# Kernel tuning notes

Measured on AMD Instinct MI355X. Metric: run time of the kernel, lower is better.

Reference implementation:

```python
import jax, jax.numpy as jnp
import numpy as np

N_NODES = 50000
N_EDGES = 800000
B, W, D, OUT = 2, 128, 64, 128


def setup_inputs() -> dict:
    key = jax.random.key(0)
    ks = jax.random.split(key, 8)
    s = lambda k, shape, fan: jax.random.normal(k, shape, dtype=jnp.float32) / np.sqrt(fan)
    return {
        "x": jax.random.normal(ks[0], (B, N_NODES, W), dtype=jnp.float32),
        "embeddings": jax.random.normal(ks[1], (N_NODES, D), dtype=jnp.float32),
        "edge_index": jax.random.randint(ks[2], (2, N_EDGES), 0, N_NODES, dtype=jnp.int64),
        "Wq": s(ks[3], (D, D), D),
        "Wk": s(ks[4], (D, D), D),
        "v": s(ks[5], (D,), D),
        "fcW": s(ks[6], (OUT, 2 * W), 2 * W),
        "fcb": jnp.zeros((OUT,), dtype=jnp.float32),
    }


def reference(x, embeddings, edge_index, Wq, Wk, v, fcW, fcb):
    B_, N, W_ = x.shape
    src, dst = edge_index[0], edge_index[1]

    # Project once on nodes, then gather per edge (same math as gather-then-linear).
    e_q = embeddings @ Wq.T        # [N, D]
    e_k = embeddings @ Wk.T        # [N, D]
    score = jnp.tanh(e_q[src] + e_k[dst]) @ v   # [E]

    # Scatter-softmax over destination nodes.
    max_vals = jax.ops.segment_max(score, dst, num_segments=N)   # [N], -inf for empty
    exp_src = jnp.exp(score - max_vals[dst])                     # [E]
    sum_exp = jax.ops.segment_sum(exp_src, dst, num_segments=N)  # [N]
    attn = exp_src / (sum_exp[dst] + 1e-8)                       # [E]

    # Weighted scatter-add aggregation of source features.
    weighted = x[:, src, :] * attn[None, :, None]                # [B, E, W]
    agg = jax.ops.segment_sum(jnp.swapaxes(weighted, 0, 1), dst, num_segments=N)  # [N, B, W]
    agg = jnp.swapaxes(agg, 0, 1)                                # [B, N, W]

    out = jnp.concatenate([x, agg], axis=-1) @ fcW.T + fcb       # [B, N, OUT]
    return jax.nn.relu(out)
```

## Files before the change

### kernel.cpp

```cpp
#include <hip/hip_runtime.h>
#include <hip/hip_bf16.h>
#include <math.h>

#define N_NODES 50000
#define N_EDGES 800000
#define BB 2
#define WFEAT 128
#define DD 64
#define OUTD 128
#define NROWS (BB * N_NODES)
#define SCAN_B 256
#define NBLK ((N_NODES + SCAN_B - 1) / SCAN_B)

#define CVTX_B 6250
#define CVTW_B 16
#define HIST_B 3125
#define PREP_B (CVTX_B + CVTW_B + HIST_B)
#define PROJ_TB ((N_NODES + 127) / 128)

typedef __attribute__((ext_vector_type(8))) short bf16x8;
typedef __attribute__((ext_vector_type(4))) float f32x4;
typedef __attribute__((ext_vector_type(2))) float f32x2;
typedef __attribute__((ext_vector_type(8))) unsigned short ushort8;

#define PRESCALE 2.8853900817779268f
#define L2E 1.4426950408889634f

static __device__ __forceinline__ unsigned short f2bf(float f) {
    __hip_bfloat16 h = __float2bfloat16(f);
    return *reinterpret_cast<unsigned short*>(&h);
}
static __device__ __forceinline__ float bf_lo(unsigned int w) {
    return __uint_as_float(w << 16);
}
static __device__ __forceinline__ float bf_hi(unsigned int w) {
    return __uint_as_float(w & 0xFFFF0000u);
}
static __device__ __forceinline__ f32x2 up2(unsigned int w) {
    f32x2 r;
    r.x = __uint_as_float(w << 16);
    r.y = __uint_as_float(w & 0xFFFF0000u);
    return r;
}
static __device__ __forceinline__ float exp2_hw(float x) {
    float r;
    asm("v_exp_f32 %0, %1" : "=v"(r) : "v"(x));
    return r;
}

__global__ __launch_bounds__(256) void prep_kernel(const float* __restrict__ x,
                                                   unsigned short* __restrict__ xb,
                                                   const float* __restrict__ fcW,
                                                   unsigned short* __restrict__ fcWb,
                                                   const int* __restrict__ dstp,
                                                   int* __restrict__ deg,
                                                   int* __restrict__ posin) {
    int bid = blockIdx.x;
    int tid = threadIdx.x;
    if (bid < CVTX_B) {
        int t = bid * 256 + tid;
        const float4* in4 = (const float4*)x;
        float4 a = in4[2 * t], b = in4[2 * t + 1];
        ushort8 o;
        o[0] = f2bf(a.x); o[1] = f2bf(a.y); o[2] = f2bf(a.z); o[3] = f2bf(a.w);
        o[4] = f2bf(b.x); o[5] = f2bf(b.y); o[6] = f2bf(b.z); o[7] = f2bf(b.w);
        *reinterpret_cast<ushort8*>(&xb[8 * t]) = o;
    } else if (bid < CVTX_B + CVTW_B) {
        int t = (bid - CVTX_B) * 256 + tid;
        const float4* in4 = (const float4*)fcW;
        float4 a = in4[2 * t], b = in4[2 * t + 1];
        ushort8 o;
        o[0] = f2bf(a.x); o[1] = f2bf(a.y); o[2] = f2bf(a.z); o[3] = f2bf(a.w);
        o[4] = f2bf(b.x); o[5] = f2bf(b.y); o[6] = f2bf(b.z); o[7] = f2bf(b.w);
        *reinterpret_cast<ushort8*>(&fcWb[8 * t]) = o;
    } else {
        int e = (bid - CVTX_B - CVTW_B) * 256 + tid;
        int d = dstp[e];
        posin[e] = atomicAdd(&deg[d], 1);
    }
}

__global__ __launch_bounds__(256) void proj_mfma(const float* __restrict__ emb,
                                                 const float* __restrict__ Wq,
                                                 const float* __restrict__ Wk,
                                                 unsigned short* __restrict__ eqb,
                                                 unsigned short* __restrict__ ekb) {
    __shared__ unsigned short As[128 * 64];
    __shared__ unsigned short Bs[128 * 64];
    int tid = threadIdx.x;
    int wave = tid >> 6, lane = tid & 63;
    int wm = wave >> 1, wn = wave & 1;
    int row0 = blockIdx.x * 128;

#pragma unroll
    for (int c = 0; c < 4; ++c) {
        int idx = (c * 256 + tid) * 8;
        int r = idx >> 6, k = idx & 63;
        int byte = (r * 128 + k * 2) ^ ((r & 7) << 4);

        int node = row0 + r;
        ushort8 o = {};
        if (node < N_NODES) {
            const float4* p = (const float4*)(emb + (size_t)node * DD + k);
            float4 a = p[0], b = p[1];
            o[0] = f2bf(a.x); o[1] = f2bf(a.y); o[2] = f2bf(a.z); o[3] = f2bf(a.w);
            o[4] = f2bf(b.x); o[5] = f2bf(b.y); o[6] = f2bf(b.z); o[7] = f2bf(b.w);
        }
        *reinterpret_cast<ushort8*>(reinterpret_cast<char*>(As) + byte) = o;

        const float* wsrc = (r < 64) ? (Wq + r * DD + k) : (Wk + (r - 64) * DD + k);
        float4 wa = *(const float4*)wsrc, wb = *((const float4*)wsrc + 1);
        ushort8 ow;
        ow[0] = f2bf(wa.x); ow[1] = f2bf(wa.y); ow[2] = f2bf(wa.z); ow[3] = f2bf(wa.w);
        ow[4] = f2bf(wb.x); ow[5] = f2bf(wb.y); ow[6] = f2bf(wb.z); ow[7] = f2bf(wb.w);
        *reinterpret_cast<ushort8*>(reinterpret_cast<char*>(Bs) + byte) = ow;
    }
    __syncthreads();

    f32x4 acc[4][4] = {};
#pragma unroll
    for (int kk = 0; kk < 2; ++kk) {
        bf16x8 a[4], b[4];
#pragma unroll
        for (int m = 0; m < 4; ++m) {
            int r = wm * 64 + m * 16 + (lane & 15);
            int k = kk * 32 + (lane >> 4) * 8;
            int byte = (r * 128 + k * 2) ^ ((r & 7) << 4);
            a[m] = *reinterpret_cast<bf16x8*>(reinterpret_cast<char*>(As) + byte);
        }
#pragma unroll
        for (int n = 0; n < 4; ++n) {
            int cn = wn * 64 + n * 16 + (lane & 15);
            int k = kk * 32 + (lane >> 4) * 8;
            int byte = (cn * 128 + k * 2) ^ ((cn & 7) << 4);
            b[n] = *reinterpret_cast<bf16x8*>(reinterpret_cast<char*>(Bs) + byte);
        }
#pragma unroll
        for (int m = 0; m < 4; ++m)
#pragma unroll
            for (int n = 0; n < 4; ++n)
                acc[m][n] = __builtin_amdgcn_mfma_f32_16x16x32_bf16(a[m], b[n], acc[m][n], 0, 0, 0);
    }

#pragma unroll
    for (int m = 0; m < 4; ++m) {
#pragma unroll
        for (int n = 0; n < 4; ++n) {
            int col = wn * 64 + n * 16 + (lane & 15);
#pragma unroll
            for (int j = 0; j < 4; ++j) {
                int row = row0 + wm * 64 + m * 16 + (lane >> 4) * 4 + j;
                if (row < N_NODES) {
                    unsigned short val = f2bf(PRESCALE * acc[m][n][j]);
                    if (col < 64) eqb[(size_t)row * DD + col] = val;
                    else          ekb[(size_t)row * DD + col - 64] = val;
                }
            }
        }
    }
}

__global__ void scan_reduce(const int* __restrict__ deg, int* __restrict__ bsum) {
    __shared__ int sh[SCAN_B];
    int i = blockIdx.x * SCAN_B + threadIdx.x;
    sh[threadIdx.x] = (i < N_NODES) ? deg[i] : 0;
    __syncthreads();
    for (int s = SCAN_B / 2; s; s >>= 1) {
        if (threadIdx.x < s) sh[threadIdx.x] += sh[threadIdx.x + s];
        __syncthreads();
    }
    if (threadIdx.x == 0) bsum[blockIdx.x] = sh[0];
}

__global__ void scan_bsum(int* __restrict__ bsum) {
    __shared__ int sh[SCAN_B];
    int tid = threadIdx.x;
    int v = (tid < NBLK) ? bsum[tid] : 0;
    sh[tid] = v;
    __syncthreads();
    for (int s = 1; s < SCAN_B; s <<= 1) {
        int t = (tid >= s) ? sh[tid - s] : 0;
        __syncthreads();
        sh[tid] += t;
        __syncthreads();
    }
    if (tid < NBLK) bsum[tid] = sh[tid] - v;
}

__global__ void scan_final(const int* __restrict__ deg, const int* __restrict__ bsum,
                           int* __restrict__ rowptr) {
    __shared__ int sh[SCAN_B];
    int i = blockIdx.x * SCAN_B + threadIdx.x;
    int v = (i < N_NODES) ? deg[i] : 0;
    sh[threadIdx.x] = v;
    __syncthreads();
    for (int s = 1; s < SCAN_B; s <<= 1) {
        int t = 0;
        if ((int)threadIdx.x >= s) t = sh[threadIdx.x - s];
        __syncthreads();
        sh[threadIdx.x] += t;
        __syncthreads();
    }
    if (i < N_NODES) {
        int excl = sh[threadIdx.x] - v + bsum[blockIdx.x];
        rowptr[i] = excl;
        if (i == N_NODES - 1) rowptr[N_NODES] = excl + v;
    }
}

__global__ void scatter_kernel(const int* __restrict__ src, const int* __restrict__ dst,
                               const int* __restrict__ rowptr, const int* __restrict__ posin,
                               int* __restrict__ src_sorted) {
    int e = blockIdx.x * blockDim.x + threadIdx.x;
    if (e >= N_EDGES) return;
    int pos = rowptr[dst[e]] + posin[e];
    src_sorted[pos] = src[e];
}

__global__ __launch_bounds__(256) void agg_fused(const unsigned short* __restrict__ eqb,
                                                 const unsigned short* __restrict__ ekb,
                                                 const float* __restrict__ v,
                                                 const unsigned short* __restrict__ xb,
                                                 const int* __restrict__ rowptr,
                                                 const int* __restrict__ src_sorted,
                                                 unsigned short* __restrict__ aggb) {
    int node = (blockIdx.x * 256 + threadIdx.x) >> 6;
    if (node >= N_NODES) return;
    int lane = threadIdx.x & 63;
    int g = lane >> 4, hl = lane & 15;

    uint2 eku = *reinterpret_cast<const uint2*>(ekb + (size_t)node * DD + 4 * hl);
    float k0 = bf_lo(eku.x), k1 = bf_hi(eku.x), k2 = bf_lo(eku.y), k3 = bf_hi(eku.y);
    float4 vv = *reinterpret_cast<const float4*>(v + 4 * hl);
    float vs = vv.x + vv.y + vv.z + vv.w;
    vs += __shfl_xor(vs, 1); vs += __shfl_xor(vs, 2);
    vs += __shfl_xor(vs, 4); vs += __shfl_xor(vs, 8);
    float vtotl2 = vs * L2E;

    int beg = rowptr[node], end = rowptr[node + 1];
    int nIter = (end - beg + 3) >> 2;

    float sum = 0.f;
    f32x2 a0[4] = {}, a1[4] = {};

    for (int i = 0; i < nIter; ++i) {
        int p = beg + 4 * i + g;
        bool valid = p < end;
        int pe = valid ? p : end - 1;
        int s = src_sorted[pe];

        uint2 equ = *reinterpret_cast<const uint2*>(eqb + (size_t)s * DD + 4 * hl);
        float s0 = bf_lo(equ.x) + k0, s1 = bf_hi(equ.x) + k1;
        float s2 = bf_lo(equ.y) + k2, s3 = bf_hi(equ.y) + k3;
        float r =      vv.x * __builtin_amdgcn_rcpf(exp2_hw(s0) + 1.f);
        r = fmaf(vv.y, __builtin_amdgcn_rcpf(exp2_hw(s1) + 1.f), r);
        r = fmaf(vv.z, __builtin_amdgcn_rcpf(exp2_hw(s2) + 1.f), r);
        r = fmaf(vv.w, __builtin_amdgcn_rcpf(exp2_hw(s3) + 1.f), r);
        r += __shfl_xor(r, 1); r += __shfl_xor(r, 2);
        r += __shfl_xor(r, 4); r += __shfl_xor(r, 8);
        float w = exp2_hw(fmaf(-2.f * L2E, r, vtotl2));
        w = valid ? w : 0.f;
        sum += w;

        uint4 u0 = *reinterpret_cast<const uint4*>(xb + (size_t)s * WFEAT + 8 * hl);
        uint4 u1 = *reinterpret_cast<const uint4*>(xb + (size_t)(N_NODES + s) * WFEAT + 8 * hl);
        a0[0] += w * up2(u0.x); a0[1] += w * up2(u0.y);
        a0[2] += w * up2(u0.z); a0[3] += w * up2(u0.w);
        a1[0] += w * up2(u1.x); a1[1] += w * up2(u1.y);
        a1[2] += w * up2(u1.z); a1[3] += w * up2(u1.w);
    }

    sum += __shfl_xor(sum, 16); sum += __shfl_xor(sum, 32);
#pragma unroll
    for (int j = 0; j < 4; ++j) {
        a0[j].x += __shfl_xor(a0[j].x, 16); a0[j].x += __shfl_xor(a0[j].x, 32);
        a0[j].y += __shfl_xor(a0[j].y, 16); a0[j].y += __shfl_xor(a0[j].y, 32);
        a1[j].x += __shfl_xor(a1[j].x, 16); a1[j].x += __shfl_xor(a1[j].x, 32);
        a1[j].y += __shfl_xor(a1[j].y, 16); a1[j].y += __shfl_xor(a1[j].y, 32);
    }
    float inv = __builtin_amdgcn_rcpf(sum + 1e-8f);

    if (g < 2) {
        float c0 = (g ? a1[0].x : a0[0].x) * inv, c1 = (g ? a1[0].y : a0[0].y) * inv;
        float c2 = (g ? a1[1].x : a0[1].x) * inv, c3 = (g ? a1[1].y : a0[1].y) * inv;
        float c4 = (g ? a1[2].x : a0[2].x) * inv, c5 = (g ? a1[2].y : a0[2].y) * inv;
        float c6 = (g ? a1[3].x : a0[3].x) * inv, c7 = (g ? a1[3].y : a0[3].y) * inv;
        uint4 o;
        o.x = (unsigned int)f2bf(c0) | ((unsigned int)f2bf(c1) << 16);
        o.y = (unsigned int)f2bf(c2) | ((unsigned int)f2bf(c3) << 16);
        o.z = (unsigned int)f2bf(c4) | ((unsigned int)f2bf(c5) << 16);
        o.w = (unsigned int)f2bf(c6) | ((unsigned int)f2bf(c7) << 16);
        size_t row = g ? (size_t)(N_NODES + node) : (size_t)node;
        *reinterpret_cast<uint4*>(&aggb[row * WFEAT + 8 * hl]) = o;
    }
}

__global__ __launch_bounds__(256) void fc_mfma(const unsigned short* __restrict__ xb,
                                               const unsigned short* __restrict__ aggb,
                                               const unsigned short* __restrict__ fcWb,
                                               const float* __restrict__ fcb,
                                               float* __restrict__ out) {
    __shared__ unsigned short As[128 * 64];
    __shared__ unsigned short Bs[128 * 64];
    int tid = threadIdx.x;
    int wave = tid >> 6, lane = tid & 63;
    int wm = wave >> 1, wn = wave & 1;
    int row0 = blockIdx.x * 128;

    f32x4 acc[4][4] = {};

    for (int ks = 0; ks < 4; ++ks) {
        const unsigned short* Asrc = (ks < 2) ? xb : aggb;
        int kbase = (ks & 1) * 64;
        __syncthreads();
#pragma unroll
        for (int c = 0; c < 4; ++c) {
            int idx = (c * 256 + tid) * 8;
            int r = idx >> 6, k = idx & 63;
            int row = row0 + r;
            ulonglong2 val = make_ulonglong2(0ull, 0ull);
            if (row < NROWS)
                val = *reinterpret_cast<const ulonglong2*>(&Asrc[(size_t)row * WFEAT + kbase + k]);
            int byte = (r * 128 + k * 2) ^ ((r & 7) << 4);
            *reinterpret_cast<ulonglong2*>(reinterpret_cast<char*>(As) + byte) = val;

            ulonglong2 wv = *reinterpret_cast<const ulonglong2*>(&fcWb[(size_t)r * 256 + ks * 64 + k]);
            *reinterpret_cast<ulonglong2*>(reinterpret_cast<char*>(Bs) + byte) = wv;
        }
        __syncthreads();
#pragma unroll
        for (int kk = 0; kk < 2; ++kk) {
            bf16x8 a[4], b[4];
#pragma unroll
            for (int m = 0; m < 4; ++m) {
                int r = wm * 64 + m * 16 + (lane & 15);
                int k = kk * 32 + (lane >> 4) * 8;
                int byte = (r * 128 + k * 2) ^ ((r & 7) << 4);
                a[m] = *reinterpret_cast<bf16x8*>(reinterpret_cast<char*>(As) + byte);
            }
#pragma unroll
            for (int n = 0; n < 4; ++n) {
                int cn = wn * 64 + n * 16 + (lane & 15);
                int k = kk * 32 + (lane >> 4) * 8;
                int byte = (cn * 128 + k * 2) ^ ((cn & 7) << 4);
                b[n] = *reinterpret_cast<bf16x8*>(reinterpret_cast<char*>(Bs) + byte);
            }
#pragma unroll
            for (int m = 0; m < 4; ++m)
#pragma unroll
                for (int n = 0; n < 4; ++n)
                    acc[m][n] = __builtin_amdgcn_mfma_f32_16x16x32_bf16(a[m], b[n], acc[m][n], 0, 0, 0);
        }
    }
#pragma unroll
    for (int m = 0; m < 4; ++m) {
#pragma unroll
        for (int n = 0; n < 4; ++n) {
            int col = wn * 64 + n * 16 + (lane & 15);
            float bias = fcb[col];
#pragma unroll
            for (int j = 0; j < 4; ++j) {
                int row = row0 + wm * 64 + m * 16 + (lane >> 4) * 4 + j;
                if (row < NROWS)
                    out[(size_t)row * OUTD + col] = fmaxf(acc[m][n][j] + bias, 0.f);
            }
        }
    }
}

extern "C" void kernel_launch(void* const* d_in, const int* in_sizes, int n_in,
                              void* d_out, int out_size, void* d_ws, size_t ws_size,
                              hipStream_t stream) {
    const float* x    = (const float*)d_in[0];
    const float* emb  = (const float*)d_in[1];
    const int*   eidx = (const int*)d_in[2];
    const float* Wq   = (const float*)d_in[3];
    const float* Wk   = (const float*)d_in[4];
    const float* v    = (const float*)d_in[5];
    const float* fcW  = (const float*)d_in[6];
    const float* fcb  = (const float*)d_in[7];
    float* out = (float*)d_out;

    char* ws = (char*)d_ws;
    unsigned short* eqb  = (unsigned short*)ws;                  ws += (size_t)N_NODES * DD * 2;
    unsigned short* ekb  = (unsigned short*)ws;                  ws += (size_t)N_NODES * DD * 2;
    unsigned short* xb   = (unsigned short*)ws;                  ws += (size_t)NROWS * WFEAT * 2;
    unsigned short* aggb = (unsigned short*)ws;                  ws += (size_t)NROWS * WFEAT * 2;
    unsigned short* fcWb = (unsigned short*)ws;                  ws += (size_t)OUTD * 256 * 2;
    int* deg        = (int*)ws;                                  ws += (size_t)N_NODES * 4;
    int* rowptr     = (int*)ws;                                  ws += (size_t)(N_NODES + 1) * 4 + 12;
    int* posin      = (int*)ws;                                  ws += (size_t)N_EDGES * 4;
    int* bsum       = (int*)ws;                                  ws += 256 * 4;
    int* src_sorted = (int*)ws;

    const int* srcp = eidx;
    const int* dstp = eidx + N_EDGES;

    hipMemsetAsync(deg, 0, (size_t)N_NODES * sizeof(int), stream);

    prep_kernel<<<PREP_B, 256, 0, stream>>>(x, xb, fcW, fcWb, dstp, deg, posin);
    proj_mfma<<<PROJ_TB, 256, 0, stream>>>(emb, Wq, Wk, eqb, ekb);
    scan_reduce<<<NBLK, SCAN_B, 0, stream>>>(deg, bsum);
    scan_bsum<<<1, SCAN_B, 0, stream>>>(bsum);
    scan_final<<<NBLK, SCAN_B, 0, stream>>>(deg, bsum, rowptr);
    scatter_kernel<<<(N_EDGES + 255) / 256, 256, 0, stream>>>(srcp, dstp, rowptr, posin,
                                                              src_sorted);
    agg_fused<<<(N_NODES * 64 + 255) / 256, 256, 0, stream>>>(eqb, ekb, v, xb, rowptr,
                                                              src_sorted, aggb);
    fc_mfma<<<(NROWS + 127) / 128, 256, 0, stream>>>(xb, aggb, fcWb, fcb, out);
}
```

Before: 186.2 us.

## Interleave batch features per node, fuse projection into prep, single-block scan, prefetch gathers

Stores the bf16 x and aggregation buffers node-major with both batches adjacent, so each source gather in the aggregation touches one contiguous 512-byte row. The embedding projection is merged into the prep kernel as extra blocks. The three-kernel scan is replaced by one 1024-thread block. The aggregation loop software-prefetches the next edge's source index, query and features. This cuts launch count and gather latency, at the cost of a serial per-thread scan loop, heavier shared memory in every prep block, and higher register pressure in the aggregation kernel.

```diff
diff --git a/kernel.cpp b/kernel.cpp
--- a/kernel.cpp
+++ b/kernel.cpp
@@ -9,14 +9,12 @@
 #define DD 64
 #define OUTD 128
 #define NROWS (BB * N_NODES)
-#define SCAN_B 256
-#define NBLK ((N_NODES + SCAN_B - 1) / SCAN_B)
-
+
+#define PROJ_TB ((N_NODES + 127) / 128)
 #define CVTX_B 6250
 #define CVTW_B 16
 #define HIST_B 3125
-#define PREP_B (CVTX_B + CVTW_B + HIST_B)
-#define PROJ_TB ((N_NODES + 127) / 128)
+#define PREP_B (PROJ_TB + CVTX_B + CVTW_B + HIST_B)
 
 typedef __attribute__((ext_vector_type(8))) short bf16x8;
 typedef __attribute__((ext_vector_type(4))) float f32x4;
@@ -48,25 +46,105 @@
     return r;
 }
 
-__global__ __launch_bounds__(256) void prep_kernel(const float* __restrict__ x,
-                                                   unsigned short* __restrict__ xb,
+__global__ __launch_bounds__(256) void prep_kernel(const float* __restrict__ emb,
+                                                   const float* __restrict__ Wq,
+                                                   const float* __restrict__ Wk,
+                                                   unsigned short* __restrict__ eqb,
+                                                   unsigned short* __restrict__ ekb,
+                                                   const float* __restrict__ x,
+                                                   unsigned short* __restrict__ xb2,
                                                    const float* __restrict__ fcW,
                                                    unsigned short* __restrict__ fcWb,
                                                    const int* __restrict__ dstp,
                                                    int* __restrict__ deg,
                                                    int* __restrict__ posin) {
+    __shared__ unsigned short As[128 * 64];
+    __shared__ unsigned short Bs[128 * 64];
     int bid = blockIdx.x;
     int tid = threadIdx.x;
-    if (bid < CVTX_B) {
-        int t = bid * 256 + tid;
+    if (bid < PROJ_TB) {
+        int wave = tid >> 6, lane = tid & 63;
+        int wm = wave >> 1, wn = wave & 1;
+        int row0 = bid * 128;
+#pragma unroll
+        for (int c = 0; c < 4; ++c) {
+            int idx = (c * 256 + tid) * 8;
+            int r = idx >> 6, k = idx & 63;
+            int byte = (r * 128 + k * 2) ^ ((r & 7) << 4);
+
+            int node = row0 + r;
+            ushort8 o = {};
+            if (node < N_NODES) {
+                const float4* p = (const float4*)(emb + (size_t)node * DD + k);
+                float4 a = p[0], b = p[1];
+                o[0] = f2bf(a.x); o[1] = f2bf(a.y); o[2] = f2bf(a.z); o[3] = f2bf(a.w);
+                o[4] = f2bf(b.x); o[5] = f2bf(b.y); o[6] = f2bf(b.z); o[7] = f2bf(b.w);
+            }
+            *reinterpret_cast<ushort8*>(reinterpret_cast<char*>(As) + byte) = o;
+
+            const float* wsrc = (r < 64) ? (Wq + r * DD + k) : (Wk + (r - 64) * DD + k);
+            float4 wa = *(const float4*)wsrc, wb = *((const float4*)wsrc + 1);
+            ushort8 ow;
+            ow[0] = f2bf(wa.x); ow[1] = f2bf(wa.y); ow[2] = f2bf(wa.z); ow[3] = f2bf(wa.w);
+            ow[4] = f2bf(wb.x); ow[5] = f2bf(wb.y); ow[6] = f2bf(wb.z); ow[7] = f2bf(wb.w);
+            *reinterpret_cast<ushort8*>(reinterpret_cast<char*>(Bs) + byte) = ow;
+        }
+        __syncthreads();
+
+        f32x4 acc[4][4] = {};
+#pragma unroll
+        for (int kk = 0; kk < 2; ++kk) {
+            bf16x8 a[4], b[4];
+#pragma unroll
+            for (int m = 0; m < 4; ++m) {
+                int r = wm * 64 + m * 16 + (lane & 15);
+                int k = kk * 32 + (lane >> 4) * 8;
+                int byte = (r * 128 + k * 2) ^ ((r & 7) << 4);
+                a[m] = *reinterpret_cast<bf16x8*>(reinterpret_cast<char*>(As) + byte);
+            }
+#pragma unroll
+            for (int n = 0; n < 4; ++n) {
+                int cn = wn * 64 + n * 16 + (lane & 15);
+                int k = kk * 32 + (lane >> 4) * 8;
+                int byte = (cn * 128 + k * 2) ^ ((cn & 7) << 4);
+                b[n] = *reinterpret_cast<bf16x8*>(reinterpret_cast<char*>(Bs) + byte);
+            }
+#pragma unroll
+            for (int m = 0; m < 4; ++m)
+#pragma unroll
+                for (int n = 0; n < 4; ++n)
+                    acc[m][n] = __builtin_amdgcn_mfma_f32_16x16x32_bf16(a[m], b[n], acc[m][n], 0, 0, 0);
+        }
+#pragma unroll
+        for (int m = 0; m < 4; ++m) {
+#pragma unroll
+            for (int n = 0; n < 4; ++n) {
+                int col = wn * 64 + n * 16 + (lane & 15);
+#pragma unroll
+                for (int j = 0; j < 4; ++j) {
+                    int row = row0 + wm * 64 + m * 16 + (lane >> 4) * 4 + j;
+                    if (row < N_NODES) {
+                        unsigned short val = f2bf(PRESCALE * acc[m][n][j]);
+                        if (col < 64) eqb[(size_t)row * DD + col] = val;
+                        else          ekb[(size_t)row * DD + col - 64] = val;
+                    }
+                }
+            }
+        }
+    } else if (bid < PROJ_TB + CVTX_B) {
+        int t = (bid - PROJ_TB) * 256 + tid;
         const float4* in4 = (const float4*)x;
         float4 a = in4[2 * t], b = in4[2 * t + 1];
         ushort8 o;
         o[0] = f2bf(a.x); o[1] = f2bf(a.y); o[2] = f2bf(a.z); o[3] = f2bf(a.w);
         o[4] = f2bf(b.x); o[5] = f2bf(b.y); o[6] = f2bf(b.z); o[7] = f2bf(b.w);
-        *reinterpret_cast<ushort8*>(&xb[8 * t]) = o;
-    } else if (bid < CVTX_B + CVTW_B) {
-        int t = (bid - CVTX_B) * 256 + tid;
+        int f0 = t * 8;
+        int bb = f0 >= N_NODES * WFEAT;
+        int rem = f0 - bb * (N_NODES * WFEAT);
+        int node = rem >> 7, feat = rem & 127;
+        *reinterpret_cast<ushort8*>(&xb2[(size_t)node * 256 + bb * 128 + feat]) = o;
+    } else if (bid < PROJ_TB + CVTX_B + CVTW_B) {
+        int t = (bid - PROJ_TB - CVTX_B) * 256 + tid;
         const float4* in4 = (const float4*)fcW;
         float4 a = in4[2 * t], b = in4[2 * t + 1];
         ushort8 o;
@@ -74,138 +152,42 @@
         o[4] = f2bf(b.x); o[5] = f2bf(b.y); o[6] = f2bf(b.z); o[7] = f2bf(b.w);
         *reinterpret_cast<ushort8*>(&fcWb[8 * t]) = o;
     } else {
-        int e = (bid - CVTX_B - CVTW_B) * 256 + tid;
+        int e = (bid - PROJ_TB - CVTX_B - CVTW_B) * 256 + tid;
         int d = dstp[e];
         posin[e] = atomicAdd(&deg[d], 1);
     }
 }
 
-__global__ __launch_bounds__(256) void proj_mfma(const float* __restrict__ emb,
-                                                 const float* __restrict__ Wq,
-                                                 const float* __restrict__ Wk,
-                                                 unsigned short* __restrict__ eqb,
-                                                 unsigned short* __restrict__ ekb) {
-    __shared__ unsigned short As[128 * 64];
-    __shared__ unsigned short Bs[128 * 64];
+#define SCAN_T 1024
+#define SCAN_C 49
+__global__ __launch_bounds__(SCAN_T) void scan_all(const int* __restrict__ deg,
+                                                   int* __restrict__ rowptr) {
+    __shared__ int part[SCAN_T];
     int tid = threadIdx.x;
-    int wave = tid >> 6, lane = tid & 63;
-    int wm = wave >> 1, wn = wave & 1;
-    int row0 = blockIdx.x * 128;
-
-#pragma unroll
-    for (int c = 0; c < 4; ++c) {
-        int idx = (c * 256 + tid) * 8;
-        int r = idx >> 6, k = idx & 63;
-        int byte = (r * 128 + k * 2) ^ ((r & 7) << 4);
-
-        int node = row0 + r;
-        ushort8 o = {};
-        if (node < N_NODES) {
-            const float4* p = (const float4*)(emb + (size_t)node * DD + k);
-            float4 a = p[0], b = p[1];
-            o[0] = f2bf(a.x); o[1] = f2bf(a.y); o[2] = f2bf(a.z); o[3] = f2bf(a.w);
-            o[4] = f2bf(b.x); o[5] = f2bf(b.y); o[6] = f2bf(b.z); o[7] = f2bf(b.w);
-        }
-        *reinterpret_cast<ushort8*>(reinterpret_cast<char*>(As) + byte) = o;
-
-        const float* wsrc = (r < 64) ? (Wq + r * DD + k) : (Wk + (r - 64) * DD + k);
-        float4 wa = *(const float4*)wsrc, wb = *((const float4*)wsrc + 1);
-        ushort8 ow;
-        ow[0] = f2bf(wa.x); ow[1] = f2bf(wa.y); ow[2] = f2bf(wa.z); ow[3] = f2bf(wa.w);
-        ow[4] = f2bf(wb.x); ow[5] = f2bf(wb.y); ow[6] = f2bf(wb.z); ow[7] = f2bf(wb.w);
-        *reinterpret_cast<ushort8*>(reinterpret_cast<char*>(Bs) + byte) = ow;
-    }
+    int base = tid * SCAN_C;
+    int s = 0;
+    for (int j = 0; j < SCAN_C; ++j) {
+        int i = base + j;
+        if (i < N_NODES) s += deg[i];
+    }
+    part[tid] = s;
     __syncthreads();
-
-    f32x4 acc[4][4] = {};
-#pragma unroll
-    for (int kk = 0; kk < 2; ++kk) {
-        bf16x8 a[4], b[4];
-#pragma unroll
-        for (int m = 0; m < 4; ++m) {
-            int r = wm * 64 + m * 16 + (lane & 15);
-            int k = kk * 32 + (lane >> 4) * 8;
-            int byte = (r * 128 + k * 2) ^ ((r & 7) << 4);
-            a[m] = *reinterpret_cast<bf16x8*>(reinterpret_cast<char*>(As) + byte);
-        }
-#pragma unroll
-        for (int n = 0; n < 4; ++n) {
-            int cn = wn * 64 + n * 16 + (lane & 15);
-            int k = kk * 32 + (lane >> 4) * 8;
-            int byte = (cn * 128 + k * 2) ^ ((cn & 7) << 4);
-            b[n] = *reinterpret_cast<bf16x8*>(reinterpret_cast<char*>(Bs) + byte);
-        }
-#pragma unroll
-        for (int m = 0; m < 4; ++m)
-#pragma unroll
-            for (int n = 0; n < 4; ++n)
-                acc[m][n] = __builtin_amdgcn_mfma_f32_16x16x32_bf16(a[m], b[n], acc[m][n], 0, 0, 0);
-    }
-
-#pragma unroll
-    for (int m = 0; m < 4; ++m) {
-#pragma unroll
-        for (int n = 0; n < 4; ++n) {
-            int col = wn * 64 + n * 16 + (lane & 15);
-#pragma unroll
-            for (int j = 0; j < 4; ++j) {
-                int row = row0 + wm * 64 + m * 16 + (lane >> 4) * 4 + j;
-                if (row < N_NODES) {
-                    unsigned short val = f2bf(PRESCALE * acc[m][n][j]);
-                    if (col < 64) eqb[(size_t)row * DD + col] = val;
-                    else          ekb[(size_t)row * DD + col - 64] = val;
-                }
-            }
-        }
-    }
-}
-
-__global__ void scan_reduce(const int* __restrict__ deg, int* __restrict__ bsum) {
-    __shared__ int sh[SCAN_B];
-    int i = blockIdx.x * SCAN_B + threadIdx.x;
-    sh[threadIdx.x] = (i < N_NODES) ? deg[i] : 0;
-    __syncthreads();
-    for (int s = SCAN_B / 2; s; s >>= 1) {
-        if (threadIdx.x < s) sh[threadIdx.x] += sh[threadIdx.x + s];
+    for (int st = 1; st < SCAN_T; st <<= 1) {
+        int t = (tid >= st) ? part[tid - st] : 0;
         __syncthreads();
-    }
-    if (threadIdx.x == 0) bsum[blockIdx.x] = sh[0];
-}
-
-__global__ void scan_bsum(int* __restrict__ bsum) {
-    __shared__ int sh[SCAN_B];
-    int tid = threadIdx.x;
-    int v = (tid < NBLK) ? bsum[tid] : 0;
-    sh[tid] = v;
-    __syncthreads();
-    for (int s = 1; s < SCAN_B; s <<= 1) {
-        int t = (tid >= s) ? sh[tid - s] : 0;
+        part[tid] += t;
         __syncthreads();
-        sh[tid] += t;
-        __syncthreads();
-    }
-    if (tid < NBLK) bsum[tid] = sh[tid] - v;
-}
-
-__global__ void scan_final(const int* __restrict__ deg, const int* __restrict__ bsum,
-                           int* __restrict__ rowptr) {
-    __shared__ int sh[SCAN_B];
-    int i = blockIdx.x * SCAN_B + threadIdx.x;
-    int v = (i < N_NODES) ? deg[i] : 0;
-    sh[threadIdx.x] = v;
-    __syncthreads();
-    for (int s = 1; s < SCAN_B; s <<= 1) {
-        int t = 0;
-        if ((int)threadIdx.x >= s) t = sh[threadIdx.x - s];
-        __syncthreads();
-        sh[threadIdx.x] += t;
-        __syncthreads();
-    }
-    if (i < N_NODES) {
-        int excl = sh[threadIdx.x] - v + bsum[blockIdx.x];
-        rowptr[i] = excl;
-        if (i == N_NODES - 1) rowptr[N_NODES] = excl + v;
-    }
+    }
+    int excl = part[tid] - s;
+    for (int j = 0; j < SCAN_C; ++j) {
+        int i = base + j;
+        if (i < N_NODES) {
+            int d = deg[i];
+            rowptr[i] = excl;
+            excl += d;
+        }
+    }
+    if (tid == SCAN_T - 1) rowptr[N_NODES] = excl;
 }
 
 __global__ void scatter_kernel(const int* __restrict__ src, const int* __restrict__ dst,
@@ -217,13 +199,17 @@
     src_sorted[pos] = src[e];
 }
 
+static __device__ __forceinline__ int pidx(int p, int beg, int end) {
+    return (p < end) ? p : ((end > beg) ? (end - 1) : 0);
+}
+
 __global__ __launch_bounds__(256) void agg_fused(const unsigned short* __restrict__ eqb,
                                                  const unsigned short* __restrict__ ekb,
                                                  const float* __restrict__ v,
-                                                 const unsigned short* __restrict__ xb,
+                                                 const unsigned short* __restrict__ xb2,
                                                  const int* __restrict__ rowptr,
                                                  const int* __restrict__ src_sorted,
-                                                 unsigned short* __restrict__ aggb) {
+                                                 unsigned short* __restrict__ aggb2) {
     int node = (blockIdx.x * 256 + threadIdx.x) >> 6;
     if (node >= N_NODES) return;
     int lane = threadIdx.x & 63;
@@ -243,13 +229,20 @@
     float sum = 0.f;
     f32x2 a0[4] = {}, a1[4] = {};
 
+    int s = src_sorted[pidx(beg + g, beg, end)];
+    uint2 equ = *reinterpret_cast<const uint2*>(eqb + (size_t)s * DD + 4 * hl);
+    const unsigned short* xr = xb2 + (size_t)s * 256 + 8 * hl;
+    uint4 u0 = *reinterpret_cast<const uint4*>(xr);
+    uint4 u1 = *reinterpret_cast<const uint4*>(xr + 128);
+
     for (int i = 0; i < nIter; ++i) {
-        int p = beg + 4 * i + g;
-        bool valid = p < end;
-        int pe = valid ? p : end - 1;
-        int s = src_sorted[pe];
-
-        uint2 equ = *reinterpret_cast<const uint2*>(eqb + (size_t)s * DD + 4 * hl);
+        bool valid = (beg + 4 * i + g) < end;
+        int sn = src_sorted[pidx(beg + 4 * (i + 1) + g, beg, end)];
+        uint2 equn = *reinterpret_cast<const uint2*>(eqb + (size_t)sn * DD + 4 * hl);
+        const unsigned short* xrn = xb2 + (size_t)sn * 256 + 8 * hl;
+        uint4 u0n = *reinterpret_cast<const uint4*>(xrn);
+        uint4 u1n = *reinterpret_cast<const uint4*>(xrn + 128);
+
         float s0 = bf_lo(equ.x) + k0, s1 = bf_hi(equ.x) + k1;
         float s2 = bf_lo(equ.y) + k2, s3 = bf_hi(equ.y) + k3;
         float r =      vv.x * __builtin_amdgcn_rcpf(exp2_hw(s0) + 1.f);
@@ -262,12 +255,12 @@
         w = valid ? w : 0.f;
         sum += w;
 
-        uint4 u0 = *reinterpret_cast<const uint4*>(xb + (size_t)s * WFEAT + 8 * hl);
-        uint4 u1 = *reinterpret_cast<const uint4*>(xb + (size_t)(N_NODES + s) * WFEAT + 8 * hl);
         a0[0] += w * up2(u0.x); a0[1] += w * up2(u0.y);
         a0[2] += w * up2(u0.z); a0[3] += w * up2(u0.w);
         a1[0] += w * up2(u1.x); a1[1] += w * up2(u1.y);
         a1[2] += w * up2(u1.z); a1[3] += w * up2(u1.w);
+
+        equ = equn; u0 = u0n; u1 = u1n;
     }
 
     sum += __shfl_xor(sum, 16); sum += __shfl_xor(sum, 32);
@@ -290,13 +283,12 @@
         o.y = (unsigned int)f2bf(c2) | ((unsigned int)f2bf(c3) << 16);
         o.z = (unsigned int)f2bf(c4) | ((unsigned int)f2bf(c5) << 16);
         o.w = (unsigned int)f2bf(c6) | ((unsigned int)f2bf(c7) << 16);
-        size_t row = g ? (size_t)(N_NODES + node) : (size_t)node;
-        *reinterpret_cast<uint4*>(&aggb[row * WFEAT + 8 * hl]) = o;
-    }
-}
-
-__global__ __launch_bounds__(256) void fc_mfma(const unsigned short* __restrict__ xb,
-                                               const unsigned short* __restrict__ aggb,
+        *reinterpret_cast<uint4*>(&aggb2[(size_t)node * 256 + (size_t)g * 128 + 8 * hl]) = o;
+    }
+}
+
+__global__ __launch_bounds__(256) void fc_mfma(const unsigned short* __restrict__ xb2,
+                                               const unsigned short* __restrict__ aggb2,
                                                const unsigned short* __restrict__ fcWb,
                                                const float* __restrict__ fcb,
                                                float* __restrict__ out) {
@@ -310,7 +302,7 @@
     f32x4 acc[4][4] = {};
 
     for (int ks = 0; ks < 4; ++ks) {
-        const unsigned short* Asrc = (ks < 2) ? xb : aggb;
+        const unsigned short* Asrc = (ks < 2) ? xb2 : aggb2;
         int kbase = (ks & 1) * 64;
         __syncthreads();
 #pragma unroll
@@ -319,8 +311,12 @@
             int r = idx >> 6, k = idx & 63;
             int row = row0 + r;
             ulonglong2 val = make_ulonglong2(0ull, 0ull);
-            if (row < NROWS)
-                val = *reinterpret_cast<const ulonglong2*>(&Asrc[(size_t)row * WFEAT + kbase + k]);
+            if (row < NROWS) {
+                int batch = row >= N_NODES;
+                int nd = row - (batch ? N_NODES : 0);
+                val = *reinterpret_cast<const ulonglong2*>(
+                        &Asrc[(size_t)nd * 256 + batch * 128 + kbase + k]);
+            }
             int byte = (r * 128 + k * 2) ^ ((r & 7) << 4);
             *reinterpret_cast<ulonglong2*>(reinterpret_cast<char*>(As) + byte) = val;
 
@@ -384,13 +380,12 @@
     char* ws = (char*)d_ws;
     unsigned short* eqb  = (unsigned short*)ws;                  ws += (size_t)N_NODES * DD * 2;
     unsigned short* ekb  = (unsigned short*)ws;                  ws += (size_t)N_NODES * DD * 2;
-    unsigned short* xb   = (unsigned short*)ws;                  ws += (size_t)NROWS * WFEAT * 2;
-    unsigned short* aggb = (unsigned short*)ws;                  ws += (size_t)NROWS * WFEAT * 2;
+    unsigned short* xb2  = (unsigned short*)ws;                  ws += (size_t)NROWS * WFEAT * 2;
+    unsigned short* aggb2= (unsigned short*)ws;                  ws += (size_t)NROWS * WFEAT * 2;
     unsigned short* fcWb = (unsigned short*)ws;                  ws += (size_t)OUTD * 256 * 2;
     int* deg        = (int*)ws;                                  ws += (size_t)N_NODES * 4;
     int* rowptr     = (int*)ws;                                  ws += (size_t)(N_NODES + 1) * 4 + 12;
     int* posin      = (int*)ws;                                  ws += (size_t)N_EDGES * 4;
-    int* bsum       = (int*)ws;                                  ws += 256 * 4;
     int* src_sorted = (int*)ws;
 
     const int* srcp = eidx;
@@ -398,14 +393,12 @@
 
     hipMemsetAsync(deg, 0, (size_t)N_NODES * sizeof(int), stream);
 
-    prep_kernel<<<PREP_B, 256, 0, stream>>>(x, xb, fcW, fcWb, dstp, deg, posin);
-    proj_mfma<<<PROJ_TB, 256, 0, stream>>>(emb, Wq, Wk, eqb, ekb);
-    scan_reduce<<<NBLK, SCAN_B, 0, stream>>>(deg, bsum);
-    scan_bsum<<<1, SCAN_B, 0, stream>>>(bsum);
-    scan_final<<<NBLK, SCAN_B, 0, stream>>>(deg, bsum, rowptr);
+    prep_kernel<<<PREP_B, 256, 0, stream>>>(emb, Wq, Wk, eqb, ekb, x, xb2, fcW, fcWb,
+                                            dstp, deg, posin);
+    scan_all<<<1, SCAN_T, 0, stream>>>(deg, rowptr);
     scatter_kernel<<<(N_EDGES + 255) / 256, 256, 0, stream>>>(srcp, dstp, rowptr, posin,
                                                               src_sorted);
-    agg_fused<<<(N_NODES * 64 + 255) / 256, 256, 0, stream>>>(eqb, ekb, v, xb, rowptr,
-                                                              src_sorted, aggb);
-    fc_mfma<<<(NROWS + 127) / 128, 256, 0, stream>>>(xb, aggb, fcWb, fcb, out);
-}
+    agg_fused<<<(N_NODES * 64 + 255) / 256, 256, 0, stream>>>(eqb, ekb, v, xb2, rowptr,
+                                                              src_sorted, aggb2);
+    fc_mfma<<<(NROWS + 127) / 128, 256, 0, stream>>>(xb2, aggb2, fcWb, fcb, out);
+}
```

New measurement: 264.0 us. 1.42x slower.
